# Kernel tuning notes

Measured on AMD Instinct MI355X. Metric: run time of the kernel, lower is better.

Reference implementation:

```python
import jax, jax.numpy as jnp
import numpy as np

N = 100000
E = 1000000
N_FEAT = 128
N_HID = 16
N_HEAD = 8
HIDDEN = N_HID * N_HEAD  # 128
N_CLASS = 64
NEG_SLOPE = 0.2


def layer_norm(x, g, b, eps=1e-5):
    mu = x.mean(-1, keepdims=True)
    var = ((x - mu) ** 2).mean(-1, keepdims=True)
    return (x - mu) * jax.lax.rsqrt(var + eps) * g + b


def gat_conv(x, src, dst, W, a_src, a_dst, bias, concat):
    # Standard GATConv math (PyG): project, per-head additive attention,
    # softmax over incoming edges (self-loops included), weighted scatter-sum.
    H, C = a_src.shape
    n = x.shape[0]
    h = (x @ W).reshape(n, H, C)                      # [N,H,C]
    al = jnp.einsum('nhc,hc->nh', h, a_src)           # [N,H]
    ar = jnp.einsum('nhc,hc->nh', h, a_dst)
    e = jax.nn.leaky_relu(al[src] + ar[dst], NEG_SLOPE)  # [E',H]
    m = jax.ops.segment_max(e, dst, num_segments=n)
    m = jnp.where(jnp.isfinite(m), m, 0.0)
    ee = jnp.exp(e - m[dst])
    den = jax.ops.segment_sum(ee, dst, num_segments=n)
    alpha = ee / (den[dst] + 1e-16)                   # [E',H]
    out = jax.ops.segment_sum(h[src] * alpha[:, :, None], dst, num_segments=n)
    out = out.reshape(n, H * C) if concat else out.mean(1)
    return out + bias, h, alpha


def setup_inputs() -> dict:
    key = jax.random.key(0)
    ks = jax.random.split(key, 20)
    s = lambda *sh: 1.0 / np.sqrt(sh[-1])
    inp = {
        'x': jax.random.normal(ks[0], (N, N_FEAT), jnp.float32),
        'edge_index': jax.random.randint(ks[1], (2, E), 0, N, jnp.int32),
        # layer 1: n_feat -> n_hid x n_head (concat)
        'W1': jax.random.normal(ks[2], (N_FEAT, HIDDEN), jnp.float32) * s(N_FEAT),
        'a_src1': jax.random.normal(ks[3], (N_HEAD, N_HID), jnp.float32) * s(N_HID),
        'a_dst1': jax.random.normal(ks[4], (N_HEAD, N_HID), jnp.float32) * s(N_HID),
        'b1': jnp.zeros((HIDDEN,), jnp.float32),
        'g1': jnp.ones((HIDDEN,), jnp.float32),
        'be1': jnp.zeros((HIDDEN,), jnp.float32),
        # layer 2: hidden -> hidden (concat)
        'W2': jax.random.normal(ks[5], (HIDDEN, HIDDEN), jnp.float32) * s(HIDDEN),
        'a_src2': jax.random.normal(ks[6], (N_HEAD, N_HID), jnp.float32) * s(N_HID),
        'a_dst2': jax.random.normal(ks[7], (N_HEAD, N_HID), jnp.float32) * s(N_HID),
        'b2': jnp.zeros((HIDDEN,), jnp.float32),
        'g2': jnp.ones((HIDDEN,), jnp.float32),
        'be2': jnp.zeros((HIDDEN,), jnp.float32),
        # out layer: hidden -> n_class, 1 head, concat=False
        'W3': jax.random.normal(ks[8], (HIDDEN, N_CLASS), jnp.float32) * s(HIDDEN),
        'a_src3': jax.random.normal(ks[9], (1, N_CLASS), jnp.float32) * s(N_CLASS),
        'a_dst3': jax.random.normal(ks[10], (1, N_CLASS), jnp.float32) * s(N_CLASS),
        'b3': jnp.zeros((N_CLASS,), jnp.float32),
        'g3': jnp.ones((N_CLASS,), jnp.float32),
        'be3': jnp.zeros((N_CLASS,), jnp.float32),
    }
    return inp


def reference(x, edge_index, W1, a_src1, a_dst1, b1, g1, be1,
              W2, a_src2, a_dst2, b2, g2, be2,
              W3, a_src3, a_dst3, b3, g3, be3):
    # add self loops (GATConv default)
    loops = jnp.arange(N, dtype=edge_index.dtype)
    src = jnp.concatenate([edge_index[0], loops])
    dst = jnp.concatenate([edge_index[1], loops])
    # Transductive path, eval mode (dropout is identity)
    x, _, _ = gat_conv(x, src, dst, W1, a_src1, a_dst1, b1, concat=True)
    x = jax.nn.elu(layer_norm(x, g1, be1))
    x, _, _ = gat_conv(x, src, dst, W2, a_src2, a_dst2, b2, concat=True)
    x = jax.nn.elu(layer_norm(x, g2, be2))
    x, _, _ = gat_conv(x, src, dst, W3, a_src3, a_dst3, b3, concat=False)
    x = layer_norm(x, g3, be3)
    return x
```

## Files before the change

### kernel.cpp

```cpp
#include <hip/hip_runtime.h>
#include <math.h>

#define N_NODES 100000
#define N_EDGES 1000000
#define EP_EDGES (N_EDGES + N_NODES)
#define NBKT ((N_NODES + 255) / 256)
#define PAD 48
#define NB_COUNT ((EP_EDGES + 4095) / 4096)
#define NB_WT ((128 * 128 + 128 * 64 + 255) / 256)

typedef short bf16x8 __attribute__((ext_vector_type(8)));
typedef float f32x4 __attribute__((ext_vector_type(4)));


__device__ inline unsigned bf16pack(float a, float b) {
    unsigned ua = __float_as_uint(a);
    unsigned ub = __float_as_uint(b);
    ua += 0x7FFFu + ((ua >> 16) & 1u);
    ub += 0x7FFFu + ((ub >> 16) & 1u);
    return (ua >> 16) | (ub & 0xFFFF0000u);
}

__device__ inline unsigned short bf16r(float a) {
    unsigned u = __float_as_uint(a);
    u += 0x7FFFu + ((u >> 16) & 1u);
    return (unsigned short)(u >> 16);
}

__device__ inline float bf16f(unsigned short v) {
    return __uint_as_float(((unsigned)v) << 16);
}

__device__ inline int swz(int o) { return o ^ (((o >> 8) & 7) << 4); }


__global__ void prep_count(const int* __restrict__ ei, int* __restrict__ bktCnt,
                           const float* __restrict__ W1, const float* __restrict__ W2,
                           const float* __restrict__ W3, unsigned short* __restrict__ Wt1,
                           unsigned short* __restrict__ Wt2, unsigned short* __restrict__ Wt3) {
    __shared__ int hist[NBKT];
    int tid = threadIdx.x;
    int b = blockIdx.x;
    if (b < NB_COUNT) {
        for (int j = tid; j < NBKT; j += 256) hist[j] = 0;
        __syncthreads();
        int e0 = b * 4096;
        int e1 = min(e0 + 4096, EP_EDGES);
        for (int e = e0 + tid; e < e1; e += 256) {
            int d = (e < N_EDGES) ? ei[N_EDGES + e] : (e - N_EDGES);
            atomicAdd(&hist[d >> 8], 1);
        }
        __syncthreads();
        for (int j = tid; j < NBKT; j += 256) {
            int c = hist[j];
            if (c) atomicAdd(&bktCnt[j], c);
        }
    } else {
        int t = (b - NB_COUNT) * 256 + tid;
        if (t < 128 * 128) {
            int k = t >> 7, c = t & 127;
            Wt1[c * 128 + k] = bf16r(W1[t]);
            Wt2[c * 128 + k] = bf16r(W2[t]);
        }
        int t3 = t - 128 * 128;
        if (t3 >= 0 && t3 < 128 * 64) {
            int k = t3 >> 6, c = t3 & 63;
            Wt3[c * 128 + k] = bf16r(W3[t3]);
        }
    }
}

__global__ void bkt_scan(const int* __restrict__ bktCnt, int* __restrict__ bktBase,
                         int* __restrict__ bktCursor) {
    __shared__ int tmp[512];
    int tid = threadIdx.x;
    int v = (tid < NBKT) ? bktCnt[tid] : 0;
    tmp[tid] = v;
    __syncthreads();
    int run = v;
    for (int off = 1; off < 512; off <<= 1) {
        int add = (tid >= off) ? tmp[tid - off] : 0;
        __syncthreads();
        run += add;
        tmp[tid] = run;
        __syncthreads();
    }
    if (tid <= NBKT) {
        int base = run - v;
        bktBase[tid] = base;
        if (tid < NBKT) bktCursor[tid] = base;
    }
}

__global__ void bkt_scatter(const int* __restrict__ ei, int* __restrict__ bktCursor,
                            unsigned* __restrict__ bktEdges) {
    __shared__ int hist[NBKT], chunk[NBKT];
    int tid = threadIdx.x;
    for (int j = tid; j < NBKT; j += 256) hist[j] = 0;
    __syncthreads();
    int e0 = blockIdx.x * 2048;
    int e1 = min(e0 + 2048, EP_EDGES);
    for (int e = e0 + tid; e < e1; e += 256) {
        int d = (e < N_EDGES) ? ei[N_EDGES + e] : (e - N_EDGES);
        atomicAdd(&hist[d >> 8], 1);
    }
    __syncthreads();
    for (int j = tid; j < NBKT; j += 256) {
        int c = hist[j];
        chunk[j] = c ? atomicAdd(&bktCursor[j], c) : 0;
        hist[j] = 0;
    }
    __syncthreads();
    for (int e = e0 + tid; e < e1; e += 256) {
        int s, d;
        if (e < N_EDGES) { s = ei[e]; d = ei[N_EDGES + e]; }
        else             { s = d = e - N_EDGES; }
        int b = d >> 8;
        int off = atomicAdd(&hist[b], 1);
        bktEdges[chunk[b] + off] = (unsigned)s | ((unsigned)(d & 255) << 24);
    }
}

__global__ void bkt_final(const unsigned* __restrict__ bktEdges, const int* __restrict__ bktBase,
                          int* __restrict__ deg_arr, int* __restrict__ pad_src) {
    __shared__ int hist[256], cur[256];
    int tid = threadIdx.x;
    int b = blockIdx.x;
    int base = bktBase[b], end = bktBase[b + 1];
    hist[tid] = 0;
    cur[tid] = 0;
    __syncthreads();
    for (int i = base + tid; i < end; i += 256)
        atomicAdd(&hist[bktEdges[i] >> 24], 1);
    __syncthreads();
    int node = b * 256 + tid;
    if (node < N_NODES) deg_arr[node] = min(hist[tid], PAD);
    __syncthreads();
    for (int i = base + tid; i < end; i += 256) {
        unsigned u = bktEdges[i];
        int d = u >> 24;
        int pos = atomicAdd(&cur[d], 1);
        if (pos < PAD)
            pad_src[(size_t)(b * 256 + d) * PAD + pos] = (int)(u & 0xFFFFFFu);
    }
    __syncthreads();
    for (int idx = tid; idx < 256 * PAD; idx += 256) {
        int dloc = idx / PAD, j = idx % PAD;
        int nd = b * 256 + dloc;
        if (nd < N_NODES && j >= min(hist[dloc], PAD))
            pad_src[(size_t)nd * PAD + j] = nd;
    }
}


template <int COUT, int H, bool IN_F32>
__launch_bounds__(256)
__global__ void gemm_mfma(const void* __restrict__ Xv, const unsigned short* __restrict__ Wt,
                          const float* __restrict__ a_src, const float* __restrict__ a_dst,
                          unsigned* __restrict__ hb16, unsigned short* __restrict__ alb,
                          float* __restrict__ ar, int n) {
    constexpr int NT = COUT / 16;
    __shared__ unsigned char lds[16384 + COUT * 256 + 1024];
    unsigned char* sx = lds;
    unsigned char* sw = lds + 16384;
    float* sc = (float*)sw;

    int tid = threadIdx.x;
    int row0 = blockIdx.x * 64;
    int lane = tid & 63;
    int wv = tid >> 6;

    if (IN_F32) {
        const float* Xf = (const float*)Xv;
        for (int c = tid; c < 1024; c += 256) {
            int o = c * 16;
            int row = o >> 8;
            int k0 = (o & 255) >> 1;
            int gr = row0 + row;
            float4 f0 = make_float4(0.f, 0.f, 0.f, 0.f), f1 = f0;
            if (gr < n) {
                f0 = *(const float4*)(Xf + (size_t)gr * 128 + k0);
                f1 = *(const float4*)(Xf + (size_t)gr * 128 + k0 + 4);
            }
            *(uint4*)(sx + swz(o)) = make_uint4(bf16pack(f0.x, f0.y), bf16pack(f0.z, f0.w),
                                                bf16pack(f1.x, f1.y), bf16pack(f1.z, f1.w));
        }
    } else {
        const unsigned char* Xb = (const unsigned char*)Xv;
        for (int c = tid; c < 1024; c += 256) {
            int o = c * 16;
            int row = o >> 8;
            int gr = row0 + row;
            uint4 v = make_uint4(0u, 0u, 0u, 0u);
            if (gr < n) v = *(const uint4*)(Xb + (size_t)gr * 256 + (o & 255));
            *(uint4*)(sx + swz(o)) = v;
        }
    }
    for (int c = tid; c < COUT * 16; c += 256) {
        int o = c * 16;
        *(uint4*)(sw + swz(o)) = *(const uint4*)((const unsigned char*)Wt + o);
    }
    __syncthreads();

    f32x4 acc[NT];
#pragma unroll
    for (int t = 0; t < NT; ++t) acc[t] = (f32x4){0.f, 0.f, 0.f, 0.f};
    int arow = wv * 16 + (lane & 15);
    int kg = lane >> 4;
#pragma unroll
    for (int s = 0; s < 4; ++s) {
        int ko = s * 64 + kg * 16;
        bf16x8 a = *(const bf16x8*)(sx + swz(arow * 256 + ko));
#pragma unroll
        for (int t = 0; t < NT; ++t) {
            bf16x8 bfr = *(const bf16x8*)(sw + swz((t * 16 + (lane & 15)) * 256 + ko));
            acc[t] = __builtin_amdgcn_mfma_f32_16x16x32_bf16(a, bfr, acc[t], 0, 0, 0);
        }
    }
    __syncthreads();

#pragma unroll
    for (int t = 0; t < NT; ++t)
#pragma unroll
        for (int i = 0; i < 4; ++i)
            sc[(wv * 16 + kg * 4 + i) * (COUT + 4) + t * 16 + (lane & 15)] = acc[t][i];
    __syncthreads();

    constexpr int NCG = COUT / 8;
    constexpr int ROWS = 64 * NCG / 256;
    int tc = tid % NCG, tr = tid / NCG;
    float asv[8], adv[8];
#pragma unroll
    for (int j = 0; j < 8; ++j) {
        asv[j] = a_src[tc * 8 + j];
        adv[j] = a_dst[tc * 8 + j];
    }
#pragma unroll
    for (int i = 0; i < ROWS; ++i) {
        int row = tr * ROWS + i;
        int gr = row0 + row;
        float h8[8];
        *(float4*)&h8[0] = *(const float4*)(sc + row * (COUT + 4) + tc * 8);
        *(float4*)&h8[4] = *(const float4*)(sc + row * (COUT + 4) + tc * 8 + 4);
        float pa = 0.f, pb = 0.f;
#pragma unroll
        for (int j = 0; j < 8; ++j) {
            pa = fmaf(h8[j], asv[j], pa);
            pb = fmaf(h8[j], adv[j], pb);
        }
        if (COUT / H == 16) {
            pa += __shfl_xor(pa, 1);
            pb += __shfl_xor(pb, 1);
            if ((tc & 1) == 0 && gr < n) {
                alb[gr * H + (tc >> 1)] = bf16r(pa);
                ar[gr * H + (tc >> 1)] = pb;
            }
        } else {
            pa += __shfl_xor(pa, 1); pb += __shfl_xor(pb, 1);
            pa += __shfl_xor(pa, 2); pb += __shfl_xor(pb, 2);
            pa += __shfl_xor(pa, 4); pb += __shfl_xor(pb, 4);
            if (tc == 0 && gr < n) {
                alb[gr] = bf16r(pa);
                ar[gr] = pb;
            }
        }
        if (gr < n) {
            *(uint4*)(hb16 + (size_t)gr * (COUT / 2) + tc * 4) =
                make_uint4(bf16pack(h8[0], h8[1]), bf16pack(h8[2], h8[3]),
                           bf16pack(h8[4], h8[5]), bf16pack(h8[6], h8[7]));
        }
    }
}


template <int H, int COUT, bool DO_ELU, bool OUTBF>
__launch_bounds__(256)
__global__ void gat_fused(const unsigned* __restrict__ hb16, const unsigned short* __restrict__ alb,
                          const float* __restrict__ ar, const int* __restrict__ deg_arr,
                          const int* __restrict__ pad_src, const float* __restrict__ bias,
                          const float* __restrict__ gamma, const float* __restrict__ beta,
                          void* __restrict__ outx, int n) {
    constexpr bool PAIR = (COUT == 128);
    __shared__ float wbuf[4][128];
    int node = blockIdx.x * 4 + (threadIdx.x >> 6);
    node = __builtin_amdgcn_readfirstlane(node);
    int l = threadIdx.x & 63;
    int wv = threadIdx.x >> 6;
    if (node >= n) return;

    int deg = deg_arr[node];
    const int* sp = pad_src + (size_t)node * PAD;
    const unsigned char* hbB = (const unsigned char*)hb16;
    const unsigned char* albB = (const unsigned char*)alb;

    float acc0 = 0.f, acc1 = 0.f, den;
    int c0 = PAIR ? 2 * l : l;

    if (PAIR) {
        unsigned loff = (unsigned)l * 4u;
        int eh = l & 7;
        int ej = l >> 3;
        int hc = l >> 3;
        float ar_e = ar[node * 8 + eh];
        bool hi = deg > 8;

        int s_lo = sp[ej];
        float a_lo = bf16f(*(const unsigned short*)(albB + (((unsigned)s_lo) << 4) + ((unsigned)eh << 1)));
        unsigned rv_lo[8];
#pragma unroll
        for (int j = 0; j < 8; ++j) {
            int sj = __builtin_amdgcn_readlane(s_lo, j * 8);
            rv_lo[j] = *(const unsigned*)(hbB + (((unsigned)sj) << 8) + loff);
        }
        float e0 = a_lo + ar_e; e0 = (e0 >= 0.f) ? e0 : 0.2f * e0;
        float w_lo = (ej < deg) ? __expf(e0) : 0.f;
        float w_hi = 0.f;
        unsigned rv_hi[8];
        if (hi) {
            int s_hi = sp[8 + ej];
            float a_hi = bf16f(*(const unsigned short*)(albB + (((unsigned)s_hi) << 4) + ((unsigned)eh << 1)));
#pragma unroll
            for (int j = 0; j < 8; ++j) {
                int sj = __builtin_amdgcn_readlane(s_hi, j * 8);
                rv_hi[j] = *(const unsigned*)(hbB + (((unsigned)sj) << 8) + loff);
            }
            float e1 = a_hi + ar_e; e1 = (e1 >= 0.f) ? e1 : 0.2f * e1;
            w_hi = (8 + ej < deg) ? __expf(e1) : 0.f;
        }
        float den_bf = w_lo + w_hi;

        *(float2*)&wbuf[wv][2 * l] = make_float2(w_lo, w_hi);
#pragma unroll
        for (int j = 0; j < 8; ++j) {
            float2 wj = *(const float2*)&wbuf[wv][2 * (j * 8 + hc)];
            acc0 = fmaf(wj.x, __uint_as_float(rv_lo[j] << 16), acc0);
            acc1 = fmaf(wj.x, __uint_as_float(rv_lo[j]), acc1);
            if (hi) {
                acc0 = fmaf(wj.y, __uint_as_float(rv_hi[j] << 16), acc0);
                acc1 = fmaf(wj.y, __uint_as_float(rv_hi[j]), acc1);
            }
        }

        for (int k = 16; k < deg; k += 8) {
            int s_c = sp[k + ej];
            float a = bf16f(*(const unsigned short*)(albB + (((unsigned)s_c) << 4) + ((unsigned)eh << 1)));
            float e = a + ar_e; e = (e >= 0.f) ? e : 0.2f * e;
            float w = (k + ej < deg) ? __expf(e) : 0.f;
            den_bf += w;
            unsigned rv[8];
#pragma unroll
            for (int j = 0; j < 8; ++j) {
                int sj = __builtin_amdgcn_readlane(s_c, j * 8);
                rv[j] = *(const unsigned*)(hbB + (((unsigned)sj) << 8) + loff);
            }
#pragma unroll
            for (int j = 0; j < 8; ++j) {
                float wj = __shfl(w, j * 8 + hc);
                acc0 = fmaf(wj, __uint_as_float(rv[j] << 16), acc0);
                acc1 = fmaf(wj, __uint_as_float(rv[j]), acc1);
            }
        }

        den_bf += __shfl_xor(den_bf, 8);
        den_bf += __shfl_xor(den_bf, 16);
        den_bf += __shfl_xor(den_bf, 32);
        den = __shfl(den_bf, hc);
    } else {
        unsigned loff2 = (unsigned)l * 2u;
        float ar_e = ar[node];
        int slot = (l < PAD) ? l : 0;
        int s_cur = sp[slot];
        float a = bf16f(*(const unsigned short*)(albB + ((unsigned)s_cur << 1)));
        float e = a + ar_e; e = (e >= 0.f) ? e : 0.2f * e;
        float w = (l < deg) ? __expf(e) : 0.f;
        float den_bf = w;
        den_bf += __shfl_xor(den_bf, 1);
        den_bf += __shfl_xor(den_bf, 2);
        den_bf += __shfl_xor(den_bf, 4);
        den_bf += __shfl_xor(den_bf, 8);
        den_bf += __shfl_xor(den_bf, 16);
        den_bf += __shfl_xor(den_bf, 32);
        den = den_bf;
        int nsub = (deg + 7) >> 3;
        for (int sub = 0; sub < nsub; ++sub) {
#pragma unroll
            for (int j2 = 0; j2 < 8; ++j2) {
                int lidx = sub * 8 + j2;
                int sj = __builtin_amdgcn_readlane(s_cur, lidx);
                float wj = __uint_as_float(__builtin_amdgcn_readlane(__float_as_uint(w), lidx));
                unsigned short rvs = *(const unsigned short*)(hbB + (((unsigned)sj) << 7) + loff2);
                acc0 = fmaf(wj, __uint_as_float(((unsigned)rvs) << 16), acc0);
            }
        }
    }

    float b0, b1v = 0.f, g0, g1v = 0.f, t0, t1v = 0.f;
    if (PAIR) {
        float2 bb = *(const float2*)(bias + c0);
        float2 gg = *(const float2*)(gamma + c0);
        float2 tt = *(const float2*)(beta + c0);
        b0 = bb.x; b1v = bb.y; g0 = gg.x; g1v = gg.y; t0 = tt.x; t1v = tt.y;
    } else {
        b0 = bias[c0]; g0 = gamma[c0]; t0 = beta[c0];
    }
    float inv = 1.f / (den + 1e-16f);
    float v0 = acc0 * inv + b0;
    float v1 = 0.f;
    float ssum = v0;
    if (PAIR) { v1 = acc1 * inv + b1v; ssum += v1; }
    for (int off = 1; off < 64; off <<= 1) ssum += __shfl_xor(ssum, off);
    float mean = ssum / COUT;
    float d0 = v0 - mean, d1 = v1 - mean;
    float vs = PAIR ? (d0 * d0 + d1 * d1) : d0 * d0;
    for (int off = 1; off < 64; off <<= 1) vs += __shfl_xor(vs, off);
    float rstd = rsqrtf(vs / COUT + 1e-5f);
    float y0 = d0 * rstd * g0 + t0;
    if (DO_ELU) y0 = (y0 > 0.f) ? y0 : (__expf(y0) - 1.f);
    if (PAIR) {
        float y1 = d1 * rstd * g1v + t1v;
        if (DO_ELU) y1 = (y1 > 0.f) ? y1 : (__expf(y1) - 1.f);
        if (OUTBF) {
            ((unsigned*)outx)[(size_t)node * 64 + l] = bf16pack(y0, y1);
        } else {
            *(float2*)((float*)outx + (size_t)node * COUT + c0) = make_float2(y0, y1);
        }
    } else {
        ((float*)outx)[(size_t)node * COUT + c0] = y0;
    }
}


extern "C" void kernel_launch(void* const* d_in, const int* in_sizes, int n_in,
                              void* d_out, int out_size, void* d_ws, size_t ws_size,
                              hipStream_t stream) {
    const float* x   = (const float*)d_in[0];
    const int*   ei  = (const int*)d_in[1];
    const float* W1  = (const float*)d_in[2];
    const float* as1 = (const float*)d_in[3];
    const float* ad1 = (const float*)d_in[4];
    const float* b1  = (const float*)d_in[5];
    const float* g1  = (const float*)d_in[6];
    const float* be1 = (const float*)d_in[7];
    const float* W2  = (const float*)d_in[8];
    const float* as2 = (const float*)d_in[9];
    const float* ad2 = (const float*)d_in[10];
    const float* b2  = (const float*)d_in[11];
    const float* g2  = (const float*)d_in[12];
    const float* be2 = (const float*)d_in[13];
    const float* W3  = (const float*)d_in[14];
    const float* as3 = (const float*)d_in[15];
    const float* ad3 = (const float*)d_in[16];
    const float* b3  = (const float*)d_in[17];
    const float* g3  = (const float*)d_in[18];
    const float* be3 = (const float*)d_in[19];
    float* out = (float*)d_out;

    char* p = (char*)d_ws;
    auto alloc = [&](size_t bytes) -> char* {
        char* r = p;
        p += (bytes + 255) & ~size_t(255);
        return r;
    };
    unsigned* hb16   = (unsigned*)alloc((size_t)N_NODES * 64 * 4);
    unsigned* xbuf   = (unsigned*)alloc((size_t)N_NODES * 64 * 4);
    unsigned short* alb = (unsigned short*)alloc((size_t)N_NODES * 8 * 2);
    float* ar        = (float*)alloc((size_t)N_NODES * 8 * 4);
    int*   deg_arr   = (int*)alloc((size_t)N_NODES * 4);
    int*   pad_src   = (int*)alloc((size_t)N_NODES * PAD * 4);
    unsigned* bktEdges = (unsigned*)alloc((size_t)EP_EDGES * 4);
    int*   bktCnt    = (int*)alloc((size_t)(NBKT + 1) * 4);
    int*   bktBase   = (int*)alloc((size_t)(NBKT + 1) * 4);
    int*   bktCursor = (int*)alloc((size_t)(NBKT + 1) * 4);
    unsigned short* Wt1 = (unsigned short*)alloc((size_t)128 * 128 * 2);
    unsigned short* Wt2 = (unsigned short*)alloc((size_t)128 * 128 * 2);
    unsigned short* Wt3 = (unsigned short*)alloc((size_t)64 * 128 * 2);

    hipMemsetAsync(bktCnt, 0, (size_t)(NBKT + 1) * 4, stream);

    prep_count<<<NB_COUNT + NB_WT, 256, 0, stream>>>(ei, bktCnt, W1, W2, W3, Wt1, Wt2, Wt3);
    bkt_scan<<<1, 512, 0, stream>>>(bktCnt, bktBase, bktCursor);
    bkt_scatter<<<(EP_EDGES + 2047) / 2048, 256, 0, stream>>>(ei, bktCursor, bktEdges);
    bkt_final<<<NBKT, 256, 0, stream>>>(bktEdges, bktBase, deg_arr, pad_src);

    const int gemm_grid = (N_NODES + 63) / 64;
    const int agg_grid  = (N_NODES + 3) / 4;

    gemm_mfma<128, 8, true><<<gemm_grid, 256, 0, stream>>>(x, Wt1, as1, ad1,
                                                           hb16, alb, ar, N_NODES);
    gat_fused<8, 128, true, true><<<agg_grid, 256, 0, stream>>>(hb16, alb, ar, deg_arr, pad_src,
                                                                b1, g1, be1, xbuf, N_NODES);
    gemm_mfma<128, 8, false><<<gemm_grid, 256, 0, stream>>>(xbuf, Wt2, as2, ad2,
                                                            hb16, alb, ar, N_NODES);
    gat_fused<8, 128, true, true><<<agg_grid, 256, 0, stream>>>(hb16, alb, ar, deg_arr, pad_src,
                                                                b2, g2, be2, xbuf, N_NODES);
    gemm_mfma<64, 1, false><<<gemm_grid, 256, 0, stream>>>(xbuf, Wt3, as3, ad3,
                                                           hb16, alb, ar, N_NODES);
    gat_fused<1, 64, false, false><<<agg_grid, 256, 0, stream>>>(hb16, alb, ar, deg_arr, pad_src,
                                                                 b3, g3, be3, out, N_NODES);
}
```

Before: 262.2 us.

## Process two nodes per wavefront with prefetched gathers in GAT aggregation

Splits the templated aggregation kernel into separate 128-wide and 64-wide kernels. Each wavefront now handles two destination nodes, issuing the first 16 neighbor gathers and attention logits for both nodes up front before computing either, so more memory loads are in flight per wave. The cost is higher register pressure from holding two nodes' row buffers, and the high-half gather is now issued unconditionally for the first node's slots, which may reduce occupancy.

```diff
diff --git a/kernel.cpp b/kernel.cpp
--- a/kernel.cpp
+++ b/kernel.cpp
@@ -273,78 +273,113 @@
 }
 
 
-template <int H, int COUT, bool DO_ELU, bool OUTBF>
 __launch_bounds__(256)
-__global__ void gat_fused(const unsigned* __restrict__ hb16, const unsigned short* __restrict__ alb,
-                          const float* __restrict__ ar, const int* __restrict__ deg_arr,
-                          const int* __restrict__ pad_src, const float* __restrict__ bias,
-                          const float* __restrict__ gamma, const float* __restrict__ beta,
-                          void* __restrict__ outx, int n) {
-    constexpr bool PAIR = (COUT == 128);
+__global__ void gat128_k(const unsigned* __restrict__ hb16, const unsigned short* __restrict__ alb,
+                         const float* __restrict__ ar, const int* __restrict__ deg_arr,
+                         const int* __restrict__ pad_src, const float* __restrict__ bias,
+                         const float* __restrict__ gamma, const float* __restrict__ beta,
+                         unsigned* __restrict__ outx, int n) {
     __shared__ float wbuf[4][128];
-    int node = blockIdx.x * 4 + (threadIdx.x >> 6);
-    node = __builtin_amdgcn_readfirstlane(node);
-    int l = threadIdx.x & 63;
-    int wv = threadIdx.x >> 6;
-    if (node >= n) return;
-
-    int deg = deg_arr[node];
-    const int* sp = pad_src + (size_t)node * PAD;
+    int tid = threadIdx.x;
+    int l = tid & 63;
+    int wv = tid >> 6;
+    int n0 = blockIdx.x * 8 + wv * 2;
+    if (n0 >= n) return;
+    bool have1 = (n0 + 1) < n;
+
+    int eh = l & 7;
+    int ej = l >> 3;
+    int hc = l >> 3;
+    unsigned loff = (unsigned)l * 4u;
     const unsigned char* hbB = (const unsigned char*)hb16;
-    const unsigned char* albB = (const unsigned char*)alb;
-
-    float acc0 = 0.f, acc1 = 0.f, den;
-    int c0 = PAIR ? 2 * l : l;
-
-    if (PAIR) {
-        unsigned loff = (unsigned)l * 4u;
-        int eh = l & 7;
-        int ej = l >> 3;
-        int hc = l >> 3;
-        float ar_e = ar[node * 8 + eh];
-        bool hi = deg > 8;
-
-        int s_lo = sp[ej];
-        float a_lo = bf16f(*(const unsigned short*)(albB + (((unsigned)s_lo) << 4) + ((unsigned)eh << 1)));
-        unsigned rv_lo[8];
+    int c0 = 2 * l;
+
+    int deg0 = deg_arr[n0];
+    int deg1 = have1 ? deg_arr[n0 + 1] : 1;
+    const int* sp0 = pad_src + (size_t)n0 * PAD;
+    const int* sp1 = sp0 + PAD;
+    int sl0 = sp0[ej], sh0 = sp0[8 + ej];
+    int sl1 = 0, sh1 = 0;
+    if (have1) { sl1 = sp1[ej]; sh1 = sp1[8 + ej]; }
+    float are0 = ar[n0 * 8 + eh];
+    float are1 = have1 ? ar[(n0 + 1) * 8 + eh] : 0.f;
+    bool hi0 = deg0 > 8, hi1 = deg1 > 8;
+
+    float a_l0 = bf16f(alb[sl0 * 8 + eh]);
+    float a_h0 = bf16f(alb[sh0 * 8 + eh]);
+    unsigned rl0[8], rh0[8];
+#pragma unroll
+    for (int j = 0; j < 8; ++j) {
+        int sj = __builtin_amdgcn_readlane(sl0, j * 8);
+        rl0[j] = *(const unsigned*)(hbB + (((unsigned)sj) << 8) + loff);
+    }
+    if (hi0) {
 #pragma unroll
         for (int j = 0; j < 8; ++j) {
-            int sj = __builtin_amdgcn_readlane(s_lo, j * 8);
-            rv_lo[j] = *(const unsigned*)(hbB + (((unsigned)sj) << 8) + loff);
-        }
-        float e0 = a_lo + ar_e; e0 = (e0 >= 0.f) ? e0 : 0.2f * e0;
+            int sj = __builtin_amdgcn_readlane(sh0, j * 8);
+            rh0[j] = *(const unsigned*)(hbB + (((unsigned)sj) << 8) + loff);
+        }
+    }
+
+    float a_l1 = 0.f, a_h1 = 0.f;
+    unsigned rl1[8], rh1[8];
+    if (have1) {
+        a_l1 = bf16f(alb[sl1 * 8 + eh]);
+        a_h1 = bf16f(alb[sh1 * 8 + eh]);
+#pragma unroll
+        for (int j = 0; j < 8; ++j) {
+            int sj = __builtin_amdgcn_readlane(sl1, j * 8);
+            rl1[j] = *(const unsigned*)(hbB + (((unsigned)sj) << 8) + loff);
+        }
+        if (hi1) {
+#pragma unroll
+            for (int j = 0; j < 8; ++j) {
+                int sj = __builtin_amdgcn_readlane(sh1, j * 8);
+                rh1[j] = *(const unsigned*)(hbB + (((unsigned)sj) << 8) + loff);
+            }
+        }
+    }
+
+    float2 bb = *(const float2*)(bias + c0);
+    float2 gg = *(const float2*)(gamma + c0);
+    float2 tt = *(const float2*)(beta + c0);
+
+#pragma unroll 1
+    for (int nd = 0; nd < 2; ++nd) {
+        if (nd == 1 && !have1) break;
+        int node  = n0 + nd;
+        int deg   = nd ? deg1 : deg0;
+        bool hi   = nd ? hi1 : hi0;
+        float a_l = nd ? a_l1 : a_l0;
+        float a_h = nd ? a_h1 : a_h0;
+        float are = nd ? are1 : are0;
+        const int* sp = nd ? sp1 : sp0;
+
+        float e0 = a_l + are; e0 = (e0 >= 0.f) ? e0 : 0.2f * e0;
         float w_lo = (ej < deg) ? __expf(e0) : 0.f;
-        float w_hi = 0.f;
-        unsigned rv_hi[8];
-        if (hi) {
-            int s_hi = sp[8 + ej];
-            float a_hi = bf16f(*(const unsigned short*)(albB + (((unsigned)s_hi) << 4) + ((unsigned)eh << 1)));
-#pragma unroll
-            for (int j = 0; j < 8; ++j) {
-                int sj = __builtin_amdgcn_readlane(s_hi, j * 8);
-                rv_hi[j] = *(const unsigned*)(hbB + (((unsigned)sj) << 8) + loff);
-            }
-            float e1 = a_hi + ar_e; e1 = (e1 >= 0.f) ? e1 : 0.2f * e1;
-            w_hi = (8 + ej < deg) ? __expf(e1) : 0.f;
-        }
+        float e1 = a_h + are; e1 = (e1 >= 0.f) ? e1 : 0.2f * e1;
+        float w_hi = (8 + ej < deg) ? __expf(e1) : 0.f;
         float den_bf = w_lo + w_hi;
 
         *(float2*)&wbuf[wv][2 * l] = make_float2(w_lo, w_hi);
+        float acc0 = 0.f, acc1 = 0.f;
 #pragma unroll
         for (int j = 0; j < 8; ++j) {
             float2 wj = *(const float2*)&wbuf[wv][2 * (j * 8 + hc)];
-            acc0 = fmaf(wj.x, __uint_as_float(rv_lo[j] << 16), acc0);
-            acc1 = fmaf(wj.x, __uint_as_float(rv_lo[j]), acc1);
+            unsigned rlv = nd ? rl1[j] : rl0[j];
+            acc0 = fmaf(wj.x, __uint_as_float(rlv << 16), acc0);
+            acc1 = fmaf(wj.x, __uint_as_float(rlv), acc1);
             if (hi) {
-                acc0 = fmaf(wj.y, __uint_as_float(rv_hi[j] << 16), acc0);
-                acc1 = fmaf(wj.y, __uint_as_float(rv_hi[j]), acc1);
+                unsigned rhv = nd ? rh1[j] : rh0[j];
+                acc0 = fmaf(wj.y, __uint_as_float(rhv << 16), acc0);
+                acc1 = fmaf(wj.y, __uint_as_float(rhv), acc1);
             }
         }
 
         for (int k = 16; k < deg; k += 8) {
             int s_c = sp[k + ej];
-            float a = bf16f(*(const unsigned short*)(albB + (((unsigned)s_c) << 4) + ((unsigned)eh << 1)));
-            float e = a + ar_e; e = (e >= 0.f) ? e : 0.2f * e;
+            float a = bf16f(alb[s_c * 8 + eh]);
+            float e = a + are; e = (e >= 0.f) ? e : 0.2f * e;
             float w = (k + ej < deg) ? __expf(e) : 0.f;
             den_bf += w;
             unsigned rv[8];
@@ -364,23 +399,77 @@
         den_bf += __shfl_xor(den_bf, 8);
         den_bf += __shfl_xor(den_bf, 16);
         den_bf += __shfl_xor(den_bf, 32);
-        den = __shfl(den_bf, hc);
-    } else {
-        unsigned loff2 = (unsigned)l * 2u;
-        float ar_e = ar[node];
-        int slot = (l < PAD) ? l : 0;
-        int s_cur = sp[slot];
-        float a = bf16f(*(const unsigned short*)(albB + ((unsigned)s_cur << 1)));
-        float e = a + ar_e; e = (e >= 0.f) ? e : 0.2f * e;
+        float den = __shfl(den_bf, hc);
+
+        float inv = 1.f / (den + 1e-16f);
+        float v0 = acc0 * inv + bb.x;
+        float v1 = acc1 * inv + bb.y;
+        float ssum = v0 + v1;
+        for (int off = 1; off < 64; off <<= 1) ssum += __shfl_xor(ssum, off);
+        float mean = ssum * (1.f / 128.f);
+        float d0 = v0 - mean, d1 = v1 - mean;
+        float vs = d0 * d0 + d1 * d1;
+        for (int off = 1; off < 64; off <<= 1) vs += __shfl_xor(vs, off);
+        float rstd = rsqrtf(vs * (1.f / 128.f) + 1e-5f);
+        float y0 = d0 * rstd * gg.x + tt.x;
+        y0 = (y0 > 0.f) ? y0 : (__expf(y0) - 1.f);
+        float y1 = d1 * rstd * gg.y + tt.y;
+        y1 = (y1 > 0.f) ? y1 : (__expf(y1) - 1.f);
+        outx[(size_t)node * 64 + l] = bf16pack(y0, y1);
+    }
+}
+
+
+__launch_bounds__(256)
+__global__ void gat64_k(const unsigned* __restrict__ hb16, const unsigned short* __restrict__ alb,
+                        const float* __restrict__ ar, const int* __restrict__ deg_arr,
+                        const int* __restrict__ pad_src, const float* __restrict__ bias,
+                        const float* __restrict__ gamma, const float* __restrict__ beta,
+                        float* __restrict__ outx, int n) {
+    int tid = threadIdx.x;
+    int l = tid & 63;
+    int wv = tid >> 6;
+    int n0 = blockIdx.x * 8 + wv * 2;
+    if (n0 >= n) return;
+    bool have1 = (n0 + 1) < n;
+
+    unsigned loff2 = (unsigned)l * 2u;
+    const unsigned char* hbB = (const unsigned char*)hb16;
+    int slot = (l < PAD) ? l : 0;
+
+    int deg0 = deg_arr[n0];
+    int deg1 = have1 ? deg_arr[n0 + 1] : 1;
+    const int* sp0 = pad_src + (size_t)n0 * PAD;
+    const int* sp1 = sp0 + PAD;
+    int sc0 = sp0[slot];
+    int sc1 = have1 ? sp1[slot] : 0;
+    float are0 = ar[n0];
+    float are1 = have1 ? ar[n0 + 1] : 0.f;
+    float a0 = bf16f(alb[sc0]);
+    float a1 = have1 ? bf16f(alb[sc1]) : 0.f;
+
+    float b0 = bias[l], g0 = gamma[l], t0 = beta[l];
+
+#pragma unroll 1
+    for (int nd = 0; nd < 2; ++nd) {
+        if (nd == 1 && !have1) break;
+        int node = n0 + nd;
+        int deg  = nd ? deg1 : deg0;
+        int s_cur = nd ? sc1 : sc0;
+        float a   = nd ? a1 : a0;
+        float are = nd ? are1 : are0;
+
+        float e = a + are; e = (e >= 0.f) ? e : 0.2f * e;
         float w = (l < deg) ? __expf(e) : 0.f;
-        float den_bf = w;
-        den_bf += __shfl_xor(den_bf, 1);
-        den_bf += __shfl_xor(den_bf, 2);
-        den_bf += __shfl_xor(den_bf, 4);
-        den_bf += __shfl_xor(den_bf, 8);
-        den_bf += __shfl_xor(den_bf, 16);
-        den_bf += __shfl_xor(den_bf, 32);
-        den = den_bf;
+        float den = w;
+        den += __shfl_xor(den, 1);
+        den += __shfl_xor(den, 2);
+        den += __shfl_xor(den, 4);
+        den += __shfl_xor(den, 8);
+        den += __shfl_xor(den, 16);
+        den += __shfl_xor(den, 32);
+
+        float acc0 = 0.f;
         int nsub = (deg + 7) >> 3;
         for (int sub = 0; sub < nsub; ++sub) {
 #pragma unroll
@@ -392,40 +481,17 @@
                 acc0 = fmaf(wj, __uint_as_float(((unsigned)rvs) << 16), acc0);
             }
         }
-    }
-
-    float b0, b1v = 0.f, g0, g1v = 0.f, t0, t1v = 0.f;
-    if (PAIR) {
-        float2 bb = *(const float2*)(bias + c0);
-        float2 gg = *(const float2*)(gamma + c0);
-        float2 tt = *(const float2*)(beta + c0);
-        b0 = bb.x; b1v = bb.y; g0 = gg.x; g1v = gg.y; t0 = tt.x; t1v = tt.y;
-    } else {
-        b0 = bias[c0]; g0 = gamma[c0]; t0 = beta[c0];
-    }
-    float inv = 1.f / (den + 1e-16f);
-    float v0 = acc0 * inv + b0;
-    float v1 = 0.f;
-    float ssum = v0;
-    if (PAIR) { v1 = acc1 * inv + b1v; ssum += v1; }
-    for (int off = 1; off < 64; off <<= 1) ssum += __shfl_xor(ssum, off);
-    float mean = ssum / COUT;
-    float d0 = v0 - mean, d1 = v1 - mean;
-    float vs = PAIR ? (d0 * d0 + d1 * d1) : d0 * d0;
-    for (int off = 1; off < 64; off <<= 1) vs += __shfl_xor(vs, off);
-    float rstd = rsqrtf(vs / COUT + 1e-5f);
-    float y0 = d0 * rstd * g0 + t0;
-    if (DO_ELU) y0 = (y0 > 0.f) ? y0 : (__expf(y0) - 1.f);
-    if (PAIR) {
-        float y1 = d1 * rstd * g1v + t1v;
-        if (DO_ELU) y1 = (y1 > 0.f) ? y1 : (__expf(y1) - 1.f);
-        if (OUTBF) {
-            ((unsigned*)outx)[(size_t)node * 64 + l] = bf16pack(y0, y1);
-        } else {
-            *(float2*)((float*)outx + (size_t)node * COUT + c0) = make_float2(y0, y1);
-        }
-    } else {
-        ((float*)outx)[(size_t)node * COUT + c0] = y0;
+
+        float inv = 1.f / (den + 1e-16f);
+        float v0 = acc0 * inv + b0;
+        float ssum = v0;
+        for (int off = 1; off < 64; off <<= 1) ssum += __shfl_xor(ssum, off);
+        float mean = ssum * (1.f / 64.f);
+        float d0 = v0 - mean;
+        float vs = d0 * d0;
+        for (int off = 1; off < 64; off <<= 1) vs += __shfl_xor(vs, off);
+        float rstd = rsqrtf(vs * (1.f / 64.f) + 1e-5f);
+        outx[(size_t)node * 64 + l] = d0 * rstd * g0 + t0;
     }
 }
 
@@ -483,18 +549,18 @@
     bkt_final<<<NBKT, 256, 0, stream>>>(bktEdges, bktBase, deg_arr, pad_src);
 
     const int gemm_grid = (N_NODES + 63) / 64;
-    const int agg_grid  = (N_NODES + 3) / 4;
+    const int agg_grid  = (N_NODES + 7) / 8;
 
     gemm_mfma<128, 8, true><<<gemm_grid, 256, 0, stream>>>(x, Wt1, as1, ad1,
                                                            hb16, alb, ar, N_NODES);
-    gat_fused<8, 128, true, true><<<agg_grid, 256, 0, stream>>>(hb16, alb, ar, deg_arr, pad_src,
-                                                                b1, g1, be1, xbuf, N_NODES);
+    gat128_k<<<agg_grid, 256, 0, stream>>>(hb16, alb, ar, deg_arr, pad_src,
+                                           b1, g1, be1, xbuf, N_NODES);
     gemm_mfma<128, 8, false><<<gemm_grid, 256, 0, stream>>>(xbuf, Wt2, as2, ad2,
                                                             hb16, alb, ar, N_NODES);
-    gat_fused<8, 128, true, true><<<agg_grid, 256, 0, stream>>>(hb16, alb, ar, deg_arr, pad_src,
-                                                                b2, g2, be2, xbuf, N_NODES);
+    gat128_k<<<agg_grid, 256, 0, stream>>>(hb16, alb, ar, deg_arr, pad_src,
+                                           b2, g2, be2, xbuf, N_NODES);
     gemm_mfma<64, 1, false><<<gemm_grid, 256, 0, stream>>>(xbuf, Wt3, as3, ad3,
                                                            hb16, alb, ar, N_NODES);
-    gat_fused<1, 64, false, false><<<agg_grid, 256, 0, stream>>>(hb16, alb, ar, deg_arr, pad_src,
-                                                                 b3, g3, be3, out, N_NODES);
-}
+    gat64_k<<<agg_grid, 256, 0, stream>>>(hb16, alb, ar, deg_arr, pad_src,
+                                          b3, g3, be3, out, N_NODES);
+}
```

Result: slower. 277.8 us (+5.9%).
